# Performance work log

Hardware: AMD Instinct MI355X
Metric: run time of the kernel (lower is better)

Reference implementation:

```python
import jax, jax.numpy as jnp
import numpy as np

B, S, D, F, E, K, T = 4, 2048, 1024, 4096, 8, 2, 64


def setup_inputs() -> dict:
    key = jax.random.key(0)
    ks = jax.random.split(key, 12)
    s = 0.02
    return {
        "inputs": jax.random.normal(ks[0], (B, S, D), jnp.float32),
        "task_param": jax.random.normal(ks[1], (B, S, T), jnp.float32),
        "alpha": jnp.array(0.5, jnp.float32),
        "Wg_in": jax.random.normal(ks[2], (D, E), jnp.float32) * s,
        "bg_in": jnp.zeros((E,), jnp.float32),
        "Wg_task": jax.random.normal(ks[3], (T, E), jnp.float32) * s,
        "bg_task": jnp.zeros((E,), jnp.float32),
        "W1": jax.random.normal(ks[4], (E, D, F), jnp.float32) * s,
        "b1": jnp.zeros((E, F), jnp.float32),
        "W2": jax.random.normal(ks[5], (E, F, D), jnp.float32) * s,
        "b2": jnp.zeros((E, D), jnp.float32),
    }


def reference(inputs, task_param, alpha, Wg_in, bg_in, Wg_task, bg_task, W1, b1, W2, b2):
    dtype = inputs.dtype
    # blended gate logits: (1-alpha)*input_gate(x) + alpha*task_gate(task)
    gate_logits = (1.0 - alpha) * (jnp.einsum("bsd,de->bse", inputs, Wg_in) + bg_in) \
                + alpha * (jnp.einsum("bst,te->bse", task_param, Wg_task) + bg_task)
    # top-k expert selection (torch.topk: sorted descending)
    topk_vals, selected = jax.lax.top_k(gate_logits, K)  # [B,S,K]
    # aux load-balancing loss
    weights_softmax = jax.nn.softmax(gate_logits.astype(jnp.float32), axis=-1).astype(dtype)
    average_weight = weights_softmax.mean(axis=(0, 1))                 # [E]
    onehot = jax.nn.one_hot(selected, E, dtype=jnp.float32)            # [B,S,K,E]
    average_count = onehot.sum(axis=2).mean(axis=(0, 1)).astype(dtype) # [E]
    l_aux = jnp.mean(average_weight * average_count) * E
    # combine weights: softmax over the K selected logits, scattered to expert slots
    w = jax.nn.softmax(topk_vals.astype(jnp.float32), axis=-1).astype(dtype)  # [B,S,K]
    combine = jnp.einsum("bsk,bske->bse", w.astype(jnp.float32), onehot).astype(dtype)  # [B,S,E]
    # dense dispatch/combine (math-equivalent to boolean-mask gather/scatter loop)
    results = jnp.zeros_like(inputs)
    for e in range(E):
        h = jax.nn.gelu(jnp.einsum("bsd,df->bsf", inputs, W1[e]) + b1[e])
        y = jnp.einsum("bsf,fd->bsd", h, W2[e]) + b2[e]
        results = results + combine[..., e:e + 1] * y
    return (results, l_aux.astype(jnp.float32))
```

## Files before the change

kernel.cpp:

```cpp
#include <hip/hip_runtime.h>

#define NTOK 8192
#define DDIM 1024
#define FDIM 4096
#define NEXP 8
#define TDIM 64
#define MAXBLK 72

#define H_OFF   (1u<<20)
#define W1B_OFF (H_OFF + 134217728u)
#define W2B_OFF (W1B_OFF + 67108864u)
#define XB_OFF  (W2B_OFF + 67108864u)
#define FULL_WS (XB_OFF + 16777216u)

typedef __bf16 bf16x8 __attribute__((ext_vector_type(8)));
typedef unsigned short u16x8 __attribute__((ext_vector_type(8)));
typedef unsigned short u16x4 __attribute__((ext_vector_type(4)));
typedef float f32x4 __attribute__((ext_vector_type(4)));

__device__ __forceinline__ float gelu_tanh(float h) {
  float u = 0.7978845608028654f * (h + 0.044715f * h * h * h);
  float e = __expf(2.0f * u);
  return 0.5f * h * (2.0f - 2.0f / (e + 1.0f));
}

__device__ __forceinline__ void glds16(const void* g, void* l) {
  __builtin_amdgcn_global_load_lds((const __attribute__((address_space(1))) void*)g,
                                   (__attribute__((address_space(3))) void*)l, 16, 0, 0);
}

__global__ __launch_bounds__(256) void gate_kernel(
    const float* __restrict__ x, const float* __restrict__ task,
    const float* __restrict__ alpha_p,
    const float* __restrict__ Wg_in, const float* __restrict__ bg_in,
    const float* __restrict__ Wg_task, const float* __restrict__ bg_task,
    int* __restrict__ cnt, float* __restrict__ wsum,
    int* __restrict__ tok_list, float* __restrict__ wt_list)
{
  __shared__ float s_wsum[NEXP];
  int tid = threadIdx.x;
  if (tid < NEXP) s_wsum[tid] = 0.0f;
  __syncthreads();

  int lane = tid & 63;
  int wid  = tid >> 6;
  int tok  = blockIdx.x * 4 + wid;
  float a  = alpha_p[0];

  const float* xr = x + (size_t)tok * DDIM;
  float accd[8] = {0,0,0,0,0,0,0,0};
#pragma unroll
  for (int i = 0; i < DDIM/64; ++i) {
    int d = lane + 64*i;
    float xv = xr[d];
    f32x4 wa = *(const f32x4*)(Wg_in + (size_t)d*8);
    f32x4 wb = *(const f32x4*)(Wg_in + (size_t)d*8 + 4);
#pragma unroll
    for (int j = 0; j < 4; ++j) {
      accd[j]   = fmaf(xv, wa[j], accd[j]);
      accd[4+j] = fmaf(xv, wb[j], accd[4+j]);
    }
  }
  float part[8];
  {
    int d = lane;
    float tv = task[(size_t)tok*TDIM + d];
    f32x4 wa = *(const f32x4*)(Wg_task + (size_t)d*8);
    f32x4 wb = *(const f32x4*)(Wg_task + (size_t)d*8 + 4);
#pragma unroll
    for (int j = 0; j < 4; ++j) {
      part[j]   = (1.0f-a)*accd[j]   + a*(tv*wa[j]);
      part[4+j] = (1.0f-a)*accd[4+j] + a*(tv*wb[j]);
    }
  }
#pragma unroll
  for (int e = 0; e < 8; ++e) {
#pragma unroll
    for (int m = 1; m < 64; m <<= 1) part[e] += __shfl_xor(part[e], m);
  }

  if (lane == 0) {
    float lg[8];
#pragma unroll
    for (int e = 0; e < 8; ++e) lg[e] = part[e] + (1.0f-a)*bg_in[e] + a*bg_task[e];
    int e0 = 0;
#pragma unroll
    for (int e = 1; e < 8; ++e) if (lg[e] > lg[e0]) e0 = e;
    int e1 = (e0 == 0) ? 1 : 0;
#pragma unroll
    for (int e = 0; e < 8; ++e) if (e != e0 && lg[e] > lg[e1]) e1 = e;
    float mx = lg[0];
#pragma unroll
    for (int e = 1; e < 8; ++e) mx = fmaxf(mx, lg[e]);
    float p[8], s = 0.0f;
#pragma unroll
    for (int e = 0; e < 8; ++e) { p[e] = __expf(lg[e] - mx); s += p[e]; }
    float inv = 1.0f / s;
#pragma unroll
    for (int e = 0; e < 8; ++e) atomicAdd(&s_wsum[e], p[e] * inv);
    float p1 = __expf(lg[e1] - lg[e0]);
    float w0 = 1.0f / (1.0f + p1);
    float w1 = p1 * w0;
    int pos0 = atomicAdd(&cnt[e0], 1);
    tok_list[e0*NTOK + pos0] = tok; wt_list[e0*NTOK + pos0] = w0;
    int pos1 = atomicAdd(&cnt[e1], 1);
    tok_list[e1*NTOK + pos1] = tok; wt_list[e1*NTOK + pos1] = w1;
  }
  __syncthreads();
  if (tid < NEXP) atomicAdd(&wsum[tid], s_wsum[tid]);
}

__global__ void finalize_kernel(const int* __restrict__ cnt, const float* __restrict__ wsum,
                                int* __restrict__ offs, float* __restrict__ laux,
                                int* __restrict__ blk_e, int* __restrict__ blk_m)
{
  if (threadIdx.x == 0) {
    int o = 0; float l = 0.0f; int nb = 0;
    for (int e = 0; e < NEXP; ++e) {
      offs[e] = o;
      for (int m0 = 0; m0 < cnt[e]; m0 += 256) {
        if (nb < MAXBLK) { blk_e[nb] = e; blk_m[nb] = m0; ++nb; }
      }
      l += (wsum[e] * (1.0f/NTOK)) * ((float)cnt[e] * (1.0f/NTOK));
      o += cnt[e];
    }
    for (; nb < MAXBLK; ++nb) blk_e[nb] = -1;
    *laux = l;
  }
}

__global__ __launch_bounds__(256) void prep_x(const float* __restrict__ X,
                                              unsigned short* __restrict__ Xb)
{
  size_t i = ((size_t)blockIdx.x*256 + threadIdx.x)*8;
  f32x4 a = *(const f32x4*)(X + i);
  f32x4 b = *(const f32x4*)(X + i + 4);
  u16x8 v;
#pragma unroll
  for (int j = 0; j < 4; ++j) {
    v[j]   = __builtin_bit_cast(unsigned short, (__bf16)a[j]);
    v[4+j] = __builtin_bit_cast(unsigned short, (__bf16)b[j]);
  }
  *(u16x8*)(Xb + i) = v;
}

template<bool PERM>
__global__ __launch_bounds__(256) void prep_w(const float* __restrict__ W,
                                              unsigned short* __restrict__ Wb,
                                              int N, int NKB, int NJ)
{
  int kb = blockIdx.x, J = blockIdx.y, e = blockIdx.z;
  int K = NKB*64;
  __shared__ unsigned short t[64*264];
  int tid = threadIdx.x;
  const float* src = W + ((size_t)e*K + (size_t)kb*64) * N + J*256;
  int k = tid >> 2, cg = tid & 3;
#pragma unroll
  for (int ii = 0; ii < 16; ++ii) {
    int n = cg*64 + ii*4;
    f32x4 v = *(const f32x4*)(src + (size_t)k*N + n);
    u16x4 b;
#pragma unroll
    for (int j = 0; j < 4; ++j) b[j] = __builtin_bit_cast(unsigned short, (__bf16)v[j]);
    *(u16x4*)&t[k*264 + n] = b;
  }
  __syncthreads();
  unsigned short* dst = Wb + ((size_t)(e*NJ + J)*NKB + kb)*16384;
#pragma unroll
  for (int i = 0; i < 8; ++i) {
    int c = i*256 + tid;
    int r = c >> 3, cc = c & 7;
    u16x8 v;
#pragma unroll
    for (int j = 0; j < 8; ++j) {
      int kloc = ((cc ^ (r&7)) << 3) + j;
      if (PERM) kloc = ((kloc & 3) << 4) | (kloc >> 2);
      v[j] = t[kloc*264 + r];
    }
    *(u16x8*)(dst + c*8) = v;
  }
}


#define STAGE(sa, sb, ks) do {                                              \
  _Pragma("unroll")                                                         \
  for (int i_ = 0; i_ < 4; ++i_) {                                          \
    glds16(asrc[i_] + (size_t)(ks)*128, (char*)(sa) + dstoff[i_]);          \
    glds16(bsrc + (size_t)(ks)*32768 + i_*8192, (char*)(sb) + dstoff[i_]);  \
  }                                                                         \
} while (0)

#define COMPUTE(sa, sb) do {                                                \
  _Pragma("unroll")                                                         \
  for (int kk_ = 0; kk_ < 2; ++kk_) {                                       \
    int csw_ = ((kk_*4 + g) ^ (q & 7)) << 3;                                \
    bf16x8 bfv_[4];                                                         \
    _Pragma("unroll")                                                       \
    for (int ni_ = 0; ni_ < 4; ++ni_)                                       \
      bfv_[ni_] = *(const bf16x8*)&(sb)[(wc*64 + ni_*16 + q)*64 + csw_];    \
    _Pragma("unroll")                                                       \
    for (int mi_ = 0; mi_ < 8; ++mi_) {                                     \
      bf16x8 af_ = *(const bf16x8*)&(sa)[(wr*128 + mi_*16 + q)*64 + csw_];  \
      _Pragma("unroll")                                                     \
      for (int ni_ = 0; ni_ < 4; ++ni_)                                     \
        acc[mi_][ni_] = __builtin_amdgcn_mfma_f32_16x16x32_bf16(af_, bfv_[ni_], acc[mi_][ni_], 0, 0, 0); \
    }                                                                       \
  }                                                                         \
} while (0)

__global__ __launch_bounds__(512) void gemm1_v4(
    const unsigned short* __restrict__ Xb, const unsigned short* __restrict__ W1b,
    const float* __restrict__ b1,
    const int* __restrict__ cnt, const int* __restrict__ offs,
    const int* __restrict__ tok_list,
    const int* __restrict__ blk_e, const int* __restrict__ blk_m,
    unsigned short* __restrict__ H)
{
  int e = blk_e[blockIdx.x];
  if (e < 0) return;
  int m0 = blk_m[blockIdx.x];
  int ce = cnt[e];
  int off = offs[e];
  int J = blockIdx.y;

  __shared__ __align__(16) unsigned short sA0[256*64], sB0[256*64];
  __shared__ __align__(16) unsigned short sA1[256*64], sB1[256*64];
  __shared__ int s_tok[256];

  int tid = threadIdx.x;
  if (tid < 256) {
    int idx = m0 + tid;
    s_tok[tid] = tok_list[e*NTOK + ((idx < ce) ? idx : (ce-1))];
  }
  __syncthreads();

  int w = tid >> 6, l = tid & 63;
  int wr = w >> 2, wc = w & 3;
  int q = l & 15, g = l >> 4;

  const char* asrc[4];
  int dstoff[4];
#pragma unroll
  for (int i = 0; i < 4; ++i) {
    int c = i*512 + tid;
    int r = c >> 3, cc = c & 7;
    asrc[i]  = (const char*)(Xb + (size_t)s_tok[r]*DDIM) + ((cc ^ (r&7)) << 4);
    dstoff[i] = c*16;
  }
  const char* bsrc = (const char*)W1b + ((size_t)(e*16 + J)*16)*32768 + (size_t)tid*16;

  f32x4 acc[8][4];
#pragma unroll
  for (int mi = 0; mi < 8; ++mi)
#pragma unroll
    for (int ni = 0; ni < 4; ++ni) acc[mi][ni] = (f32x4){0.f,0.f,0.f,0.f};

  STAGE(sA0, sB0, 0);
  asm volatile("s_waitcnt vmcnt(0)" ::: "memory");
  __builtin_amdgcn_s_barrier();

#define NK1 (DDIM/64)
  for (int ks = 0; ks < NK1; ks += 2) {
    STAGE(sA1, sB1, ks+1);
    COMPUTE(sA0, sB0);
    asm volatile("s_waitcnt vmcnt(0)" ::: "memory");
    __builtin_amdgcn_s_barrier();
    if (ks + 2 < NK1) STAGE(sA0, sB0, ks+2);
    COMPUTE(sA1, sB1);
    asm volatile("s_waitcnt vmcnt(0)" ::: "memory");
    __builtin_amdgcn_s_barrier();
  }

  int n0 = J*256;
  float bias[4];
#pragma unroll
  for (int ni = 0; ni < 4; ++ni) bias[ni] = b1[(size_t)e*FDIM + n0 + wc*64 + ni*16 + q];
#pragma unroll
  for (int mi = 0; mi < 8; ++mi) {
#pragma unroll
    for (int j = 0; j < 4; ++j) {
      int r = wr*128 + mi*16 + g*4 + j;
      if (m0 + r >= ce) continue;
      u16x4 hv;
#pragma unroll
      for (int ni = 0; ni < 4; ++ni) {
        float h = acc[mi][ni][j] + bias[ni];
        hv[ni] = __builtin_bit_cast(unsigned short, (__bf16)gelu_tanh(h));
      }
      *(u16x4*)&H[(size_t)(off + m0 + r)*FDIM + n0 + wc*64 + q*4] = hv;
    }
  }
}

__global__ __launch_bounds__(512) void gemm2_v4(
    const unsigned short* __restrict__ H, const unsigned short* __restrict__ W2b,
    const float* __restrict__ b2,
    const int* __restrict__ cnt, const int* __restrict__ offs,
    const int* __restrict__ tok_list, const float* __restrict__ wt_list,
    const int* __restrict__ blk_e, const int* __restrict__ blk_m,
    float* __restrict__ out)
{
  int e = blk_e[blockIdx.x];
  if (e < 0) return;
  int m0 = blk_m[blockIdx.x];
  int ce = cnt[e];
  int off = offs[e];
  int J = blockIdx.y;

  __shared__ __align__(16) unsigned short sA0[256*64], sB0[256*64];
  __shared__ __align__(16) unsigned short sA1[256*64], sB1[256*64];
  __shared__ int   s_tok[256];
  __shared__ float s_wt[256];

  int tid = threadIdx.x;
  if (tid < 256) {
    int idx = m0 + tid;
    int cidx = (idx < ce) ? idx : (ce-1);
    s_tok[tid] = tok_list[e*NTOK + cidx];
    s_wt[tid]  = (idx < ce) ? wt_list[e*NTOK + cidx] : 0.0f;
  }
  __syncthreads();

  int w = tid >> 6, l = tid & 63;
  int wr = w >> 2, wc = w & 3;
  int q = l & 15, g = l >> 4;

  const char* asrc[4];
  int dstoff[4];
#pragma unroll
  for (int i = 0; i < 4; ++i) {
    int c = i*512 + tid;
    int r = c >> 3, cc = c & 7;
    int rr = (m0 + r < ce) ? r : (ce-1-m0);
    asrc[i]  = (const char*)(H + (size_t)(off + m0 + rr)*FDIM) + ((cc ^ (r&7)) << 4);
    dstoff[i] = c*16;
  }
  const char* bsrc = (const char*)W2b + ((size_t)(e*4 + J)*64)*32768 + (size_t)tid*16;

  f32x4 acc[8][4];
#pragma unroll
  for (int mi = 0; mi < 8; ++mi)
#pragma unroll
    for (int ni = 0; ni < 4; ++ni) acc[mi][ni] = (f32x4){0.f,0.f,0.f,0.f};

  STAGE(sA0, sB0, 0);
  asm volatile("s_waitcnt vmcnt(0)" ::: "memory");
  __builtin_amdgcn_s_barrier();

#define NK2 (FDIM/64)
  for (int ks = 0; ks < NK2; ks += 2) {
    STAGE(sA1, sB1, ks+1);
    COMPUTE(sA0, sB0);
    asm volatile("s_waitcnt vmcnt(0)" ::: "memory");
    __builtin_amdgcn_s_barrier();
    if (ks + 2 < NK2) STAGE(sA0, sB0, ks+2);
    COMPUTE(sA1, sB1);
    asm volatile("s_waitcnt vmcnt(0)" ::: "memory");
    __builtin_amdgcn_s_barrier();
  }

  int n0 = J*256;
  float bias[4];
#pragma unroll
  for (int ni = 0; ni < 4; ++ni) bias[ni] = b2[(size_t)e*DDIM + n0 + wc*64 + ni*16 + q];
#pragma unroll
  for (int mi = 0; mi < 8; ++mi) {
#pragma unroll
    for (int j = 0; j < 4; ++j) {
      int r = wr*128 + mi*16 + g*4 + j;
      if (m0 + r >= ce) continue;
      int tok = s_tok[r];
      float wt = s_wt[r];
      float* orow = out + (size_t)tok * DDIM;
#pragma unroll
      for (int ni = 0; ni < 4; ++ni) {
        float y = acc[mi][ni][j] + bias[ni];
        unsafeAtomicAdd(&orow[n0 + wc*64 + ni*16 + q], wt * y);
      }
    }
  }
}

extern "C" void kernel_launch(void* const* d_in, const int* in_sizes, int n_in,
                              void* d_out, int out_size, void* d_ws, size_t ws_size,
                              hipStream_t stream)
{
  const float* x       = (const float*)d_in[0];
  const float* task    = (const float*)d_in[1];
  const float* alpha   = (const float*)d_in[2];
  const float* Wg_in   = (const float*)d_in[3];
  const float* bg_in   = (const float*)d_in[4];
  const float* Wg_task = (const float*)d_in[5];
  const float* bg_task = (const float*)d_in[6];
  const float* W1      = (const float*)d_in[7];
  const float* b1      = (const float*)d_in[8];
  const float* W2      = (const float*)d_in[9];
  const float* b2      = (const float*)d_in[10];
  float* out = (float*)d_out;

  char* ws = (char*)d_ws;
  int*   cnt      = (int*)(ws + 0);
  float* wsum     = (float*)(ws + 32);
  int*   offs     = (int*)(ws + 64);
  int*   blk_e    = (int*)(ws + 128);
  int*   blk_m    = (int*)(ws + 512);
  int*   tok_list = (int*)(ws + 4096);
  float* wt_list  = (float*)(ws + 4096 + NTOK*NEXP*4);
  unsigned short* H   = (unsigned short*)(ws + H_OFF);
  unsigned short* W1b = (unsigned short*)(ws + W1B_OFF);
  unsigned short* W2b = (unsigned short*)(ws + W2B_OFF);
  unsigned short* Xb  = (unsigned short*)(ws + XB_OFF);

  hipMemsetAsync(d_out, 0, (size_t)out_size * sizeof(float), stream);
  hipMemsetAsync(ws, 0, 128, stream);
  gate_kernel<<<NTOK/4, 256, 0, stream>>>(x, task, alpha, Wg_in, bg_in, Wg_task, bg_task,
                                          cnt, wsum, tok_list, wt_list);
  finalize_kernel<<<1, 64, 0, stream>>>(cnt, wsum, offs, out + (size_t)NTOK*DDIM, blk_e, blk_m);
  prep_x<<<NTOK*DDIM/2048, 256, 0, stream>>>(x, Xb);
  prep_w<false><<<dim3(16, 16, NEXP), 256, 0, stream>>>(W1, W1b, FDIM, 16, 16);
  prep_w<true ><<<dim3(64,  4, NEXP), 256, 0, stream>>>(W2, W2b, DDIM, 64, 4);
  gemm1_v4<<<dim3(MAXBLK, FDIM/256), 512, 0, stream>>>(Xb, W1b, b1, cnt, offs, tok_list,
                                                       blk_e, blk_m, H);
  gemm2_v4<<<dim3(MAXBLK, DDIM/256), 512, 0, stream>>>(H, W2b, b2, cnt, offs, tok_list, wt_list,
                                                       blk_e, blk_m, out);
}
```

Baseline: 821.8 us.

## Switch expert GEMMs to 4-stage K=32 pipeline with split-K for GEMM2

Both grouped GEMMs move from a double-buffered K=64 loop that waits for all loads each step to a four-buffer ring of K=32 tiles, using partial vmcnt waits so up to three stages stay in flight. The weight pre-pack and the A-tile gather are re-laid out so two rows share one swizzled 64-element LDS line. The kernels also raise wave priority around the MFMA bursts and swap grid axes so blocks sharing a row tile launch together. GEMM2 gains a split-K of 2 along F, doubling the block count for better CU occupancy at the cost of twice as many atomic adds to the output.

```diff
diff --git a/kernel.cpp b/kernel.cpp
--- a/kernel.cpp
+++ b/kernel.cpp
@@ -28,6 +28,11 @@
   __builtin_amdgcn_global_load_lds((const __attribute__((address_space(1))) void*)g,
                                    (__attribute__((address_space(3))) void*)l, 16, 0, 0);
 }
+
+#define VM8() asm volatile("s_waitcnt vmcnt(8)" ::: "memory")
+#define VM4() asm volatile("s_waitcnt vmcnt(4)" ::: "memory")
+#define VM0() asm volatile("s_waitcnt vmcnt(0)" ::: "memory")
+#define BAR() __builtin_amdgcn_s_barrier()
 
 __global__ __launch_bounds__(256) void gate_kernel(
     const float* __restrict__ x, const float* __restrict__ task,
@@ -168,47 +173,53 @@
   unsigned short* dst = Wb + ((size_t)(e*NJ + J)*NKB + kb)*16384;
 #pragma unroll
   for (int i = 0; i < 8; ++i) {
-    int c = i*256 + tid;
-    int r = c >> 3, cc = c & 7;
+    int c2 = i*256 + tid;
+    int cl = c2 & 1023;
+    int h  = c2 >> 10;
+    int R  = cl >> 3, dp = cl & 7;
+    int d  = dp ^ (R & 7);
+    int nloc = (R<<1) | (d>>2);
+    int pbase = h*32 + (d&3)*8;
     u16x8 v;
 #pragma unroll
     for (int j = 0; j < 8; ++j) {
-      int kloc = ((cc ^ (r&7)) << 3) + j;
-      if (PERM) kloc = ((kloc & 3) << 4) | (kloc >> 2);
-      v[j] = t[kloc*264 + r];
-    }
-    *(u16x8*)(dst + c*8) = v;
-  }
-}
-
-
-#define STAGE(sa, sb, ks) do {                                              \
-  _Pragma("unroll")                                                         \
-  for (int i_ = 0; i_ < 4; ++i_) {                                          \
-    glds16(asrc[i_] + (size_t)(ks)*128, (char*)(sa) + dstoff[i_]);          \
-    glds16(bsrc + (size_t)(ks)*32768 + i_*8192, (char*)(sb) + dstoff[i_]);  \
-  }                                                                         \
+      int v64 = pbase + j;
+      int kl  = PERM ? (((v64 & 3) << 4) | (v64 >> 2)) : v64;
+      v[j] = t[kl*264 + nloc];
+    }
+    *(u16x8*)(dst + (size_t)c2*8) = v;
+  }
+}
+
+
+#define STAGE(bufbase, t) do {                                                \
+  char* sa__ = ldsb + (bufbase);                                              \
+  _Pragma("unroll")                                                           \
+  for (int i_ = 0; i_ < 2; ++i_) {                                            \
+    glds16(asrc[i_] + (size_t)(t)*64, sa__ + dstoff[i_]);                     \
+    glds16(bsrc + (size_t)(t)*16384 + i_*8192, sa__ + 16384 + dstoff[i_]);    \
+  }                                                                           \
 } while (0)
 
-#define COMPUTE(sa, sb) do {                                                \
-  _Pragma("unroll")                                                         \
-  for (int kk_ = 0; kk_ < 2; ++kk_) {                                       \
-    int csw_ = ((kk_*4 + g) ^ (q & 7)) << 3;                                \
-    bf16x8 bfv_[4];                                                         \
-    _Pragma("unroll")                                                       \
-    for (int ni_ = 0; ni_ < 4; ++ni_)                                       \
-      bfv_[ni_] = *(const bf16x8*)&(sb)[(wc*64 + ni_*16 + q)*64 + csw_];    \
-    _Pragma("unroll")                                                       \
-    for (int mi_ = 0; mi_ < 8; ++mi_) {                                     \
-      bf16x8 af_ = *(const bf16x8*)&(sa)[(wr*128 + mi_*16 + q)*64 + csw_];  \
-      _Pragma("unroll")                                                     \
-      for (int ni_ = 0; ni_ < 4; ++ni_)                                     \
-        acc[mi_][ni_] = __builtin_amdgcn_mfma_f32_16x16x32_bf16(af_, bfv_[ni_], acc[mi_][ni_], 0, 0, 0); \
-    }                                                                       \
-  }                                                                         \
+#define COMPUTE(bufbase) do {                                                 \
+  const unsigned short* sa_ = (const unsigned short*)(ldsb + (bufbase));      \
+  const unsigned short* sb_ = sa_ + 8192;                                     \
+  bf16x8 bfv_[4];                                                             \
+  _Pragma("unroll")                                                           \
+  for (int ni_ = 0; ni_ < 4; ++ni_)                                           \
+    bfv_[ni_] = *(const bf16x8*)&sb_[boff0 + ni_*512];                        \
+  __builtin_amdgcn_s_setprio(1);                                              \
+  _Pragma("unroll")                                                           \
+  for (int mi_ = 0; mi_ < 8; ++mi_) {                                         \
+    bf16x8 af_ = *(const bf16x8*)&sa_[aoff0 + mi_*512];                       \
+    _Pragma("unroll")                                                         \
+    for (int ni_ = 0; ni_ < 4; ++ni_)                                         \
+      acc[mi_][ni_] = __builtin_amdgcn_mfma_f32_16x16x32_bf16(af_, bfv_[ni_], acc[mi_][ni_], 0, 0, 0); \
+  }                                                                           \
+  __builtin_amdgcn_s_setprio(0);                                              \
 } while (0)
 
-__global__ __launch_bounds__(512) void gemm1_v4(
+__global__ __launch_bounds__(512) void gemm1_v5(
     const unsigned short* __restrict__ Xb, const unsigned short* __restrict__ W1b,
     const float* __restrict__ b1,
     const int* __restrict__ cnt, const int* __restrict__ offs,
@@ -216,15 +227,14 @@
     const int* __restrict__ blk_e, const int* __restrict__ blk_m,
     unsigned short* __restrict__ H)
 {
-  int e = blk_e[blockIdx.x];
+  int e = blk_e[blockIdx.y];
   if (e < 0) return;
-  int m0 = blk_m[blockIdx.x];
+  int m0 = blk_m[blockIdx.y];
   int ce = cnt[e];
   int off = offs[e];
-  int J = blockIdx.y;
-
-  __shared__ __align__(16) unsigned short sA0[256*64], sB0[256*64];
-  __shared__ __align__(16) unsigned short sA1[256*64], sB1[256*64];
+  int J = blockIdx.x;
+
+  __shared__ __align__(16) char ldsb[131072];
   __shared__ int s_tok[256];
 
   int tid = threadIdx.x;
@@ -234,20 +244,29 @@
   }
   __syncthreads();
 
-  int w = tid >> 6, l = tid & 63;
+  int l = tid & 63, w = tid >> 6;
   int wr = w >> 2, wc = w & 3;
   int q = l & 15, g = l >> 4;
 
-  const char* asrc[4];
-  int dstoff[4];
-#pragma unroll
-  for (int i = 0; i < 4; ++i) {
+  const char* asrc[2];
+  int dstoff[2];
+#pragma unroll
+  for (int i = 0; i < 2; ++i) {
     int c = i*512 + tid;
-    int r = c >> 3, cc = c & 7;
-    asrc[i]  = (const char*)(Xb + (size_t)s_tok[r]*DDIM) + ((cc ^ (r&7)) << 4);
+    int R = c >> 3, dp = c & 7;
+    int d = dp ^ (R & 7);
+    int r = (R << 1) | (d >> 2);
+    int kc = d & 3;
+    asrc[i] = (const char*)(Xb + (size_t)s_tok[r]*DDIM) + kc*16;
     dstoff[i] = c*16;
   }
-  const char* bsrc = (const char*)W1b + ((size_t)(e*16 + J)*16)*32768 + (size_t)tid*16;
+  const char* bsrc = (const char*)W1b + (size_t)((e*16 + J)*32) * 16384 + (size_t)tid*16;
+
+  int rowA = wr*128 + q, rowB = wc*64 + q;
+  int RA = rowA >> 1, RB = rowB >> 1;
+  int dq = ((q & 1) << 2) | g;
+  const int aoff0 = RA*64 + (dq ^ (RA & 7))*8;
+  const int boff0 = RB*64 + (dq ^ (RB & 7))*8;
 
   f32x4 acc[8][4];
 #pragma unroll
@@ -255,21 +274,17 @@
 #pragma unroll
     for (int ni = 0; ni < 4; ++ni) acc[mi][ni] = (f32x4){0.f,0.f,0.f,0.f};
 
-  STAGE(sA0, sB0, 0);
-  asm volatile("s_waitcnt vmcnt(0)" ::: "memory");
-  __builtin_amdgcn_s_barrier();
-
-#define NK1 (DDIM/64)
-  for (int ks = 0; ks < NK1; ks += 2) {
-    STAGE(sA1, sB1, ks+1);
-    COMPUTE(sA0, sB0);
-    asm volatile("s_waitcnt vmcnt(0)" ::: "memory");
-    __builtin_amdgcn_s_barrier();
-    if (ks + 2 < NK1) STAGE(sA0, sB0, ks+2);
-    COMPUTE(sA1, sB1);
-    asm volatile("s_waitcnt vmcnt(0)" ::: "memory");
-    __builtin_amdgcn_s_barrier();
-  }
+#define NT1 (DDIM/32)
+  STAGE(0, 0); STAGE(32768, 1); STAGE(65536, 2);
+  VM8(); BAR();
+  for (int t = 0; t < NT1-3; ++t) {
+    STAGE(((t+3)&3)*32768, t+3);
+    COMPUTE((t&3)*32768);
+    VM8(); BAR();
+  }
+  COMPUTE(((NT1-3)&3)*32768); VM4(); BAR();
+  COMPUTE(((NT1-2)&3)*32768); VM0(); BAR();
+  COMPUTE(((NT1-1)&3)*32768);
 
   int n0 = J*256;
   float bias[4];
@@ -292,7 +307,7 @@
   }
 }
 
-__global__ __launch_bounds__(512) void gemm2_v4(
+__global__ __launch_bounds__(512) void gemm2_v5(
     const unsigned short* __restrict__ H, const unsigned short* __restrict__ W2b,
     const float* __restrict__ b2,
     const int* __restrict__ cnt, const int* __restrict__ offs,
@@ -300,15 +315,15 @@
     const int* __restrict__ blk_e, const int* __restrict__ blk_m,
     float* __restrict__ out)
 {
-  int e = blk_e[blockIdx.x];
+  int e = blk_e[blockIdx.y];
   if (e < 0) return;
-  int m0 = blk_m[blockIdx.x];
+  int m0 = blk_m[blockIdx.y];
   int ce = cnt[e];
   int off = offs[e];
-  int J = blockIdx.y;
-
-  __shared__ __align__(16) unsigned short sA0[256*64], sB0[256*64];
-  __shared__ __align__(16) unsigned short sA1[256*64], sB1[256*64];
+  int J = blockIdx.x;
+  int s = blockIdx.z;
+
+  __shared__ __align__(16) char ldsb[131072];
   __shared__ int   s_tok[256];
   __shared__ float s_wt[256];
 
@@ -321,21 +336,30 @@
   }
   __syncthreads();
 
-  int w = tid >> 6, l = tid & 63;
+  int l = tid & 63, w = tid >> 6;
   int wr = w >> 2, wc = w & 3;
   int q = l & 15, g = l >> 4;
 
-  const char* asrc[4];
-  int dstoff[4];
-#pragma unroll
-  for (int i = 0; i < 4; ++i) {
+  const char* asrc[2];
+  int dstoff[2];
+#pragma unroll
+  for (int i = 0; i < 2; ++i) {
     int c = i*512 + tid;
-    int r = c >> 3, cc = c & 7;
+    int R = c >> 3, dp = c & 7;
+    int d = dp ^ (R & 7);
+    int r = (R << 1) | (d >> 2);
+    int kc = d & 3;
     int rr = (m0 + r < ce) ? r : (ce-1-m0);
-    asrc[i]  = (const char*)(H + (size_t)(off + m0 + rr)*FDIM) + ((cc ^ (r&7)) << 4);
+    asrc[i] = (const char*)(H + (size_t)(off + m0 + rr)*FDIM) + kc*16 + s*4096;
     dstoff[i] = c*16;
   }
-  const char* bsrc = (const char*)W2b + ((size_t)(e*4 + J)*64)*32768 + (size_t)tid*16;
+  const char* bsrc = (const char*)W2b + (size_t)((e*4 + J)*128 + s*64) * 16384 + (size_t)tid*16;
+
+  int rowA = wr*128 + q, rowB = wc*64 + q;
+  int RA = rowA >> 1, RB = rowB >> 1;
+  int dq = ((q & 1) << 2) | g;
+  const int aoff0 = RA*64 + (dq ^ (RA & 7))*8;
+  const int boff0 = RB*64 + (dq ^ (RB & 7))*8;
 
   f32x4 acc[8][4];
 #pragma unroll
@@ -343,26 +367,23 @@
 #pragma unroll
     for (int ni = 0; ni < 4; ++ni) acc[mi][ni] = (f32x4){0.f,0.f,0.f,0.f};
 
-  STAGE(sA0, sB0, 0);
-  asm volatile("s_waitcnt vmcnt(0)" ::: "memory");
-  __builtin_amdgcn_s_barrier();
-
-#define NK2 (FDIM/64)
-  for (int ks = 0; ks < NK2; ks += 2) {
-    STAGE(sA1, sB1, ks+1);
-    COMPUTE(sA0, sB0);
-    asm volatile("s_waitcnt vmcnt(0)" ::: "memory");
-    __builtin_amdgcn_s_barrier();
-    if (ks + 2 < NK2) STAGE(sA0, sB0, ks+2);
-    COMPUTE(sA1, sB1);
-    asm volatile("s_waitcnt vmcnt(0)" ::: "memory");
-    __builtin_amdgcn_s_barrier();
-  }
+#define NT2 (FDIM/32/2)
+  STAGE(0, 0); STAGE(32768, 1); STAGE(65536, 2);
+  VM8(); BAR();
+  for (int t = 0; t < NT2-3; ++t) {
+    STAGE(((t+3)&3)*32768, t+3);
+    COMPUTE((t&3)*32768);
+    VM8(); BAR();
+  }
+  COMPUTE(((NT2-3)&3)*32768); VM4(); BAR();
+  COMPUTE(((NT2-2)&3)*32768); VM0(); BAR();
+  COMPUTE(((NT2-1)&3)*32768);
 
   int n0 = J*256;
   float bias[4];
 #pragma unroll
-  for (int ni = 0; ni < 4; ++ni) bias[ni] = b2[(size_t)e*DDIM + n0 + wc*64 + ni*16 + q];
+  for (int ni = 0; ni < 4; ++ni)
+    bias[ni] = (s == 0) ? b2[(size_t)e*DDIM + n0 + wc*64 + ni*16 + q] : 0.0f;
 #pragma unroll
   for (int mi = 0; mi < 8; ++mi) {
 #pragma unroll
@@ -419,8 +440,8 @@
   prep_x<<<NTOK*DDIM/2048, 256, 0, stream>>>(x, Xb);
   prep_w<false><<<dim3(16, 16, NEXP), 256, 0, stream>>>(W1, W1b, FDIM, 16, 16);
   prep_w<true ><<<dim3(64,  4, NEXP), 256, 0, stream>>>(W2, W2b, DDIM, 64, 4);
-  gemm1_v4<<<dim3(MAXBLK, FDIM/256), 512, 0, stream>>>(Xb, W1b, b1, cnt, offs, tok_list,
-                                                       blk_e, blk_m, H);
-  gemm2_v4<<<dim3(MAXBLK, DDIM/256), 512, 0, stream>>>(H, W2b, b2, cnt, offs, tok_list, wt_list,
-                                                       blk_e, blk_m, out);
-}
+  gemm1_v5<<<dim3(16, MAXBLK), 512, 0, stream>>>(Xb, W1b, b1, cnt, offs, tok_list,
+                                                 blk_e, blk_m, H);
+  gemm2_v5<<<dim3(4, MAXBLK, 2), 512, 0, stream>>>(H, W2b, b2, cnt, offs, tok_list, wt_list,
+                                                   blk_e, blk_m, out);
+}
```

After: 911.6 us. 1.11x slower.

## Split gemm2 K dimension across two blocks and pre-gather expert tokens

Applied to the files above, without the earlier changes.

The second expert GEMM now splits the F reduction into two halves across a new grid z dimension. The two halves are summed through the existing atomic adds, and only the first half adds the bias. This doubles the block count to improve CU occupancy when few expert tiles exist, at the cost of twice the atomic traffic to the output. When the workspace is large enough, a new gather kernel also writes bf16 copies of the routed tokens contiguously in expert order, so gemm1 reads rows linearly instead of through an indirect token lookup.

```diff
diff --git a/kernel.cpp b/kernel.cpp
--- a/kernel.cpp
+++ b/kernel.cpp
@@ -12,6 +12,7 @@
 #define W2B_OFF (W1B_OFF + 67108864u)
 #define XB_OFF  (W2B_OFF + 67108864u)
 #define FULL_WS (XB_OFF + 16777216u)
+#define WS_BIG  (XB_OFF + 33554432u)
 
 typedef __bf16 bf16x8 __attribute__((ext_vector_type(8)));
 typedef unsigned short u16x8 __attribute__((ext_vector_type(8)));
@@ -144,6 +145,30 @@
   *(u16x8*)(Xb + i) = v;
 }
 
+__global__ __launch_bounds__(256) void prep_gather(
+    const float* __restrict__ X,
+    const int* __restrict__ offs, const int* __restrict__ tok_list,
+    unsigned short* __restrict__ Xg)
+{
+  int tid = threadIdx.x;
+  int sl = blockIdx.x*2 + (tid >> 7);
+  int e = 0;
+#pragma unroll
+  for (int k = 1; k < NEXP; ++k) if (sl >= offs[k]) e = k;
+  int tok = tok_list[e*NTOK + (sl - offs[e])];
+  int c8 = (tid & 127) * 8;
+  const float* src = X + (size_t)tok * DDIM + c8;
+  f32x4 a = *(const f32x4*)(src);
+  f32x4 b = *(const f32x4*)(src + 4);
+  u16x8 v;
+#pragma unroll
+  for (int j = 0; j < 4; ++j) {
+    v[j]   = __builtin_bit_cast(unsigned short, (__bf16)a[j]);
+    v[4+j] = __builtin_bit_cast(unsigned short, (__bf16)b[j]);
+  }
+  *(u16x8*)(Xg + (size_t)sl * DDIM + c8) = v;
+}
+
 template<bool PERM>
 __global__ __launch_bounds__(256) void prep_w(const float* __restrict__ W,
                                               unsigned short* __restrict__ Wb,
@@ -173,9 +198,9 @@
     u16x8 v;
 #pragma unroll
     for (int j = 0; j < 8; ++j) {
-      int kloc = ((cc ^ (r&7)) << 3) + j;
-      if (PERM) kloc = ((kloc & 3) << 4) | (kloc >> 2);
-      v[j] = t[kloc*264 + r];
+      int v64 = (cc ^ (r&7))*8 + j;
+      int kl  = PERM ? (((v64 & 3) << 4) | (v64 >> 2)) : v64;
+      v[j] = t[kl*264 + r];
     }
     *(u16x8*)(dst + c*8) = v;
   }
@@ -208,8 +233,9 @@
   }                                                                         \
 } while (0)
 
-__global__ __launch_bounds__(512) void gemm1_v4(
-    const unsigned short* __restrict__ Xb, const unsigned short* __restrict__ W1b,
+template<bool LIN>
+__global__ __launch_bounds__(512) void gemm1_v8(
+    const unsigned short* __restrict__ Xsrc, const unsigned short* __restrict__ W1b,
     const float* __restrict__ b1,
     const int* __restrict__ cnt, const int* __restrict__ offs,
     const int* __restrict__ tok_list,
@@ -228,11 +254,13 @@
   __shared__ int s_tok[256];
 
   int tid = threadIdx.x;
-  if (tid < 256) {
-    int idx = m0 + tid;
-    s_tok[tid] = tok_list[e*NTOK + ((idx < ce) ? idx : (ce-1))];
-  }
-  __syncthreads();
+  if (!LIN) {
+    if (tid < 256) {
+      int idx = m0 + tid;
+      s_tok[tid] = tok_list[e*NTOK + ((idx < ce) ? idx : (ce-1))];
+    }
+    __syncthreads();
+  }
 
   int w = tid >> 6, l = tid & 63;
   int wr = w >> 2, wc = w & 3;
@@ -244,7 +272,12 @@
   for (int i = 0; i < 4; ++i) {
     int c = i*512 + tid;
     int r = c >> 3, cc = c & 7;
-    asrc[i]  = (const char*)(Xb + (size_t)s_tok[r]*DDIM) + ((cc ^ (r&7)) << 4);
+    if (LIN) {
+      int rr = (m0 + r < ce) ? r : (ce-1-m0);
+      asrc[i] = (const char*)(Xsrc + (size_t)(off + m0 + rr)*DDIM) + ((cc ^ (r&7)) << 4);
+    } else {
+      asrc[i] = (const char*)(Xsrc + (size_t)s_tok[r]*DDIM) + ((cc ^ (r&7)) << 4);
+    }
     dstoff[i] = c*16;
   }
   const char* bsrc = (const char*)W1b + ((size_t)(e*16 + J)*16)*32768 + (size_t)tid*16;
@@ -292,7 +325,7 @@
   }
 }
 
-__global__ __launch_bounds__(512) void gemm2_v4(
+__global__ __launch_bounds__(512) void gemm2_v8(
     const unsigned short* __restrict__ H, const unsigned short* __restrict__ W2b,
     const float* __restrict__ b2,
     const int* __restrict__ cnt, const int* __restrict__ offs,
@@ -306,6 +339,7 @@
   int ce = cnt[e];
   int off = offs[e];
   int J = blockIdx.y;
+  int s = blockIdx.z;
 
   __shared__ __align__(16) unsigned short sA0[256*64], sB0[256*64];
   __shared__ __align__(16) unsigned short sA1[256*64], sB1[256*64];
@@ -332,10 +366,10 @@
     int c = i*512 + tid;
     int r = c >> 3, cc = c & 7;
     int rr = (m0 + r < ce) ? r : (ce-1-m0);
-    asrc[i]  = (const char*)(H + (size_t)(off + m0 + rr)*FDIM) + ((cc ^ (r&7)) << 4);
+    asrc[i]  = (const char*)(H + (size_t)(off + m0 + rr)*FDIM) + ((cc ^ (r&7)) << 4) + s*4096;
     dstoff[i] = c*16;
   }
-  const char* bsrc = (const char*)W2b + ((size_t)(e*4 + J)*64)*32768 + (size_t)tid*16;
+  const char* bsrc = (const char*)W2b + ((size_t)(e*4 + J)*64 + s*32)*32768 + (size_t)tid*16;
 
   f32x4 acc[8][4];
 #pragma unroll
@@ -347,7 +381,7 @@
   asm volatile("s_waitcnt vmcnt(0)" ::: "memory");
   __builtin_amdgcn_s_barrier();
 
-#define NK2 (FDIM/64)
+#define NK2 (FDIM/64/2)
   for (int ks = 0; ks < NK2; ks += 2) {
     STAGE(sA1, sB1, ks+1);
     COMPUTE(sA0, sB0);
@@ -362,7 +396,8 @@
   int n0 = J*256;
   float bias[4];
 #pragma unroll
-  for (int ni = 0; ni < 4; ++ni) bias[ni] = b2[(size_t)e*DDIM + n0 + wc*64 + ni*16 + q];
+  for (int ni = 0; ni < 4; ++ni)
+    bias[ni] = (s == 0) ? b2[(size_t)e*DDIM + n0 + wc*64 + ni*16 + q] : 0.0f;
 #pragma unroll
   for (int mi = 0; mi < 8; ++mi) {
 #pragma unroll
@@ -410,17 +445,25 @@
   unsigned short* W1b = (unsigned short*)(ws + W1B_OFF);
   unsigned short* W2b = (unsigned short*)(ws + W2B_OFF);
   unsigned short* Xb  = (unsigned short*)(ws + XB_OFF);
+  unsigned short* Xg  = (unsigned short*)(ws + XB_OFF);
 
   hipMemsetAsync(d_out, 0, (size_t)out_size * sizeof(float), stream);
   hipMemsetAsync(ws, 0, 128, stream);
   gate_kernel<<<NTOK/4, 256, 0, stream>>>(x, task, alpha, Wg_in, bg_in, Wg_task, bg_task,
                                           cnt, wsum, tok_list, wt_list);
   finalize_kernel<<<1, 64, 0, stream>>>(cnt, wsum, offs, out + (size_t)NTOK*DDIM, blk_e, blk_m);
-  prep_x<<<NTOK*DDIM/2048, 256, 0, stream>>>(x, Xb);
   prep_w<false><<<dim3(16, 16, NEXP), 256, 0, stream>>>(W1, W1b, FDIM, 16, 16);
   prep_w<true ><<<dim3(64,  4, NEXP), 256, 0, stream>>>(W2, W2b, DDIM, 64, 4);
-  gemm1_v4<<<dim3(MAXBLK, FDIM/256), 512, 0, stream>>>(Xb, W1b, b1, cnt, offs, tok_list,
-                                                       blk_e, blk_m, H);
-  gemm2_v4<<<dim3(MAXBLK, DDIM/256), 512, 0, stream>>>(H, W2b, b2, cnt, offs, tok_list, wt_list,
-                                                       blk_e, blk_m, out);
-}
+
+  if (ws_size >= (size_t)WS_BIG) {
+    prep_gather<<<NTOK, 256, 0, stream>>>(x, offs, tok_list, Xg);
+    gemm1_v8<true><<<dim3(MAXBLK, FDIM/256), 512, 0, stream>>>(Xg, W1b, b1, cnt, offs,
+                                                               tok_list, blk_e, blk_m, H);
+  } else {
+    prep_x<<<NTOK*DDIM/2048, 256, 0, stream>>>(x, Xb);
+    gemm1_v8<false><<<dim3(MAXBLK, FDIM/256), 512, 0, stream>>>(Xb, W1b, b1, cnt, offs,
+                                                                tok_list, blk_e, blk_m, H);
+  }
+  gemm2_v8<<<dim3(MAXBLK, DDIM/256, 2), 512, 0, stream>>>(H, W2b, b2, cnt, offs, tok_list,
+                                                          wt_list, blk_e, blk_m, out);
+}
```

New measurement: 850.0 us. 3.4% more time.

## Pre-gather tokens into tiled layout, shrink K-tiles, split-K gemm2 for occupancy

Applied to the files above, without the earlier changes.

Replaces the flat bf16 conversion of X with a kernel that gathers routed tokens into pre-swizzled, tile-contiguous blocks. Both GEMMs can then stage A and B with fully contiguous global-to-LDS loads. K-tiles drop from 64 to 32, cutting LDS per block and allowing launch_bounds(512,4) for higher occupancy. GEMM1 writes H directly in the tiled layout GEMM2 consumes, and GEMM2 is split along K into two halves that accumulate through the existing atomics, doubling grid parallelism. The cost is twice as many barrier-synchronised K iterations, an extra gather pass over X, and twice as many atomic adds in the gemm2 epilogue.

```diff
diff --git a/kernel.cpp b/kernel.cpp
--- a/kernel.cpp
+++ b/kernel.cpp
@@ -7,11 +7,11 @@
 #define TDIM 64
 #define MAXBLK 72
 
-#define H_OFF   (1u<<20)
-#define W1B_OFF (H_OFF + 134217728u)
-#define W2B_OFF (W1B_OFF + 67108864u)
-#define XB_OFF  (W2B_OFF + 67108864u)
-#define FULL_WS (XB_OFF + 16777216u)
+#define HG_OFF   1048576u
+#define W1B_OFF  (HG_OFF + 150994944u)
+#define W2B_OFF  (W1B_OFF + 67108864u)
+#define XGT_OFF  (W2B_OFF + 67108864u)
+#define WS_NEED  (XGT_OFF + 37748736u)
 
 typedef __bf16 bf16x8 __attribute__((ext_vector_type(8)));
 typedef unsigned short u16x8 __attribute__((ext_vector_type(8)));
@@ -28,6 +28,9 @@
   __builtin_amdgcn_global_load_lds((const __attribute__((address_space(1))) void*)g,
                                    (__attribute__((address_space(3))) void*)l, 16, 0, 0);
 }
+
+#define VM0() asm volatile("s_waitcnt vmcnt(0)" ::: "memory")
+#define SBAR() __syncthreads()
 
 __global__ __launch_bounds__(256) void gate_kernel(
     const float* __restrict__ x, const float* __restrict__ task,
@@ -129,21 +132,6 @@
   }
 }
 
-__global__ __launch_bounds__(256) void prep_x(const float* __restrict__ X,
-                                              unsigned short* __restrict__ Xb)
-{
-  size_t i = ((size_t)blockIdx.x*256 + threadIdx.x)*8;
-  f32x4 a = *(const f32x4*)(X + i);
-  f32x4 b = *(const f32x4*)(X + i + 4);
-  u16x8 v;
-#pragma unroll
-  for (int j = 0; j < 4; ++j) {
-    v[j]   = __builtin_bit_cast(unsigned short, (__bf16)a[j]);
-    v[4+j] = __builtin_bit_cast(unsigned short, (__bf16)b[j]);
-  }
-  *(u16x8*)(Xb + i) = v;
-}
-
 template<bool PERM>
 __global__ __launch_bounds__(256) void prep_w(const float* __restrict__ W,
                                               unsigned short* __restrict__ Wb,
@@ -165,89 +153,129 @@
     *(u16x4*)&t[k*264 + n] = b;
   }
   __syncthreads();
-  unsigned short* dst = Wb + ((size_t)(e*NJ + J)*NKB + kb)*16384;
+  unsigned short* dst = Wb + ((size_t)(e*NJ + J)*NKB + kb) * 16384;
 #pragma unroll
   for (int i = 0; i < 8; ++i) {
-    int c = i*256 + tid;
-    int r = c >> 3, cc = c & 7;
+    int c2 = i*256 + tid;
+    int h  = c2 >> 10, cl = c2 & 1023;
+    int R  = cl >> 3, dp = cl & 7;
+    int d  = dp ^ (R & 7);
+    int n  = (R << 1) | (d >> 2);
+    int kb8 = (d & 3) * 8;
     u16x8 v;
 #pragma unroll
     for (int j = 0; j < 8; ++j) {
-      int kloc = ((cc ^ (r&7)) << 3) + j;
-      if (PERM) kloc = ((kloc & 3) << 4) | (kloc >> 2);
-      v[j] = t[kloc*264 + r];
-    }
-    *(u16x8*)(dst + c*8) = v;
-  }
-}
-
-
-#define STAGE(sa, sb, ks) do {                                              \
-  _Pragma("unroll")                                                         \
-  for (int i_ = 0; i_ < 4; ++i_) {                                          \
-    glds16(asrc[i_] + (size_t)(ks)*128, (char*)(sa) + dstoff[i_]);          \
-    glds16(bsrc + (size_t)(ks)*32768 + i_*8192, (char*)(sb) + dstoff[i_]);  \
-  }                                                                         \
-} while (0)
-
-#define COMPUTE(sa, sb) do {                                                \
-  _Pragma("unroll")                                                         \
-  for (int kk_ = 0; kk_ < 2; ++kk_) {                                       \
-    int csw_ = ((kk_*4 + g) ^ (q & 7)) << 3;                                \
-    bf16x8 bfv_[4];                                                         \
-    _Pragma("unroll")                                                       \
-    for (int ni_ = 0; ni_ < 4; ++ni_)                                       \
-      bfv_[ni_] = *(const bf16x8*)&(sb)[(wc*64 + ni_*16 + q)*64 + csw_];    \
-    _Pragma("unroll")                                                       \
-    for (int mi_ = 0; mi_ < 8; ++mi_) {                                     \
-      bf16x8 af_ = *(const bf16x8*)&(sa)[(wr*128 + mi_*16 + q)*64 + csw_];  \
-      _Pragma("unroll")                                                     \
-      for (int ni_ = 0; ni_ < 4; ++ni_)                                     \
-        acc[mi_][ni_] = __builtin_amdgcn_mfma_f32_16x16x32_bf16(af_, bfv_[ni_], acc[mi_][ni_], 0, 0, 0); \
-    }                                                                       \
-  }                                                                         \
-} while (0)
-
-__global__ __launch_bounds__(512) void gemm1_v4(
-    const unsigned short* __restrict__ Xb, const unsigned short* __restrict__ W1b,
-    const float* __restrict__ b1,
-    const int* __restrict__ cnt, const int* __restrict__ offs,
-    const int* __restrict__ tok_list,
+      int vv = h*32 + kb8 + j;
+      int sk = PERM ? (((vv & 3) << 4) | (vv >> 2)) : vv;
+      v[j] = t[sk*264 + n];
+    }
+    *(u16x8*)(dst + (size_t)c2*8) = v;
+  }
+}
+
+__global__ __launch_bounds__(256) void prep_gather_t(
+    const float* __restrict__ X,
+    const int* __restrict__ cnt, const int* __restrict__ tok_list,
     const int* __restrict__ blk_e, const int* __restrict__ blk_m,
-    unsigned short* __restrict__ H)
-{
-  int e = blk_e[blockIdx.x];
+    unsigned short* __restrict__ XgT)
+{
+  int kt = blockIdx.x, bi = blockIdx.y;
+  int e = blk_e[bi];
   if (e < 0) return;
-  int m0 = blk_m[blockIdx.x];
-  int ce = cnt[e];
-  int off = offs[e];
-  int J = blockIdx.y;
-
-  __shared__ __align__(16) unsigned short sA0[256*64], sB0[256*64];
-  __shared__ __align__(16) unsigned short sA1[256*64], sB1[256*64];
+  int m0 = blk_m[bi], ce = cnt[e];
   __shared__ int s_tok[256];
-
   int tid = threadIdx.x;
   if (tid < 256) {
     int idx = m0 + tid;
     s_tok[tid] = tok_list[e*NTOK + ((idx < ce) ? idx : (ce-1))];
   }
   __syncthreads();
-
+  unsigned short* dst = XgT + ((size_t)bi*32 + kt) * 8192;
+#pragma unroll
+  for (int i = 0; i < 4; ++i) {
+    int c = i*256 + tid;
+    int R = c >> 3, dp = c & 7;
+    int d = dp ^ (R & 7);
+    int row = (R << 1) | (d >> 2);
+    int kloc = (d & 3) * 8;
+    const float* src = X + (size_t)s_tok[row]*DDIM + kt*32 + kloc;
+    f32x4 a = *(const f32x4*)(src);
+    f32x4 b = *(const f32x4*)(src + 4);
+    u16x8 v;
+#pragma unroll
+    for (int j = 0; j < 4; ++j) {
+      v[j]   = __builtin_bit_cast(unsigned short, (__bf16)a[j]);
+      v[4+j] = __builtin_bit_cast(unsigned short, (__bf16)b[j]);
+    }
+    *(u16x8*)(dst + (size_t)c*8) = v;
+  }
+}
+
+
+#define STAGE(sa, sb, kt) do {                                                 \
+  glds16(abase + (size_t)(kt)*16384 + t16,        (char*)(sa) + t16);          \
+  glds16(abase + (size_t)(kt)*16384 + 8192 + t16, (char*)(sa) + 8192 + t16);   \
+  glds16(bbase + (size_t)(kt)*16384 + t16,        (char*)(sb) + t16);          \
+  glds16(bbase + (size_t)(kt)*16384 + 8192 + t16, (char*)(sb) + 8192 + t16);   \
+} while (0)
+
+#define COMPUTE(sa, sb) do {                                                   \
+  bf16x8 bfv_[4];                                                              \
+  _Pragma("unroll")                                                            \
+  for (int ni_ = 0; ni_ < 4; ++ni_)                                            \
+    bfv_[ni_] = *(const bf16x8*)&(sb)[boff0 + ni_*512];                        \
+  _Pragma("unroll")                                                            \
+  for (int mi_ = 0; mi_ < 8; ++mi_) {                                          \
+    bf16x8 af_ = *(const bf16x8*)&(sa)[aoff0 + mi_*512];                       \
+    _Pragma("unroll")                                                          \
+    for (int ni_ = 0; ni_ < 4; ++ni_)                                          \
+      acc[mi_][ni_] = __builtin_amdgcn_mfma_f32_16x16x32_bf16(                 \
+          af_, bfv_[ni_], acc[mi_][ni_], 0, 0, 0);                             \
+  }                                                                            \
+} while (0)
+
+#define KLOOP(NT) do {                                                         \
+  STAGE(sA0, sB0, 0);                                                          \
+  VM0(); SBAR();                                                               \
+  for (int kt = 0; kt < (NT); kt += 2) {                                       \
+    STAGE(sA1, sB1, kt+1);                                                     \
+    COMPUTE(sA0, sB0);                                                         \
+    VM0(); SBAR();                                                             \
+    if (kt + 2 < (NT)) STAGE(sA0, sB0, kt+2);                                  \
+    COMPUTE(sA1, sB1);                                                         \
+    VM0(); SBAR();                                                             \
+  }                                                                            \
+} while (0)
+
+__global__ __launch_bounds__(512, 4) void gemm1_v11(
+    const unsigned short* __restrict__ XgT, const unsigned short* __restrict__ W1b,
+    const float* __restrict__ b1,
+    const int* __restrict__ cnt,
+    const int* __restrict__ blk_e, const int* __restrict__ blk_m,
+    unsigned short* __restrict__ Hg)
+{
+  int J = blockIdx.x;
+  int bi = blockIdx.y;
+  int e = blk_e[bi];
+  if (e < 0) return;
+  int m0 = blk_m[bi];
+  int ce = cnt[e];
+
+  __shared__ __align__(16) unsigned short sA0[8192], sB0[8192], sA1[8192], sB1[8192];
+
+  int tid = threadIdx.x;
   int w = tid >> 6, l = tid & 63;
   int wr = w >> 2, wc = w & 3;
   int q = l & 15, g = l >> 4;
-
-  const char* asrc[4];
-  int dstoff[4];
-#pragma unroll
-  for (int i = 0; i < 4; ++i) {
-    int c = i*512 + tid;
-    int r = c >> 3, cc = c & 7;
-    asrc[i]  = (const char*)(Xb + (size_t)s_tok[r]*DDIM) + ((cc ^ (r&7)) << 4);
-    dstoff[i] = c*16;
-  }
-  const char* bsrc = (const char*)W1b + ((size_t)(e*16 + J)*16)*32768 + (size_t)tid*16;
+  const int t16 = tid * 16;
+
+  const char* abase = (const char*)XgT + (size_t)bi * 524288;
+  const char* bbase = (const char*)W1b + (size_t)(e*16 + J) * 32 * 16384;
+
+  int hq = q >> 1;
+  int swz = ((((q & 1) << 2) | g) ^ (hq & 7));
+  const int aoff0 = (wr*64 + hq)*64 + swz*8;
+  const int boff0 = (wc*32 + hq)*64 + swz*8;
 
   f32x4 acc[8][4];
 #pragma unroll
@@ -255,22 +283,12 @@
 #pragma unroll
     for (int ni = 0; ni < 4; ++ni) acc[mi][ni] = (f32x4){0.f,0.f,0.f,0.f};
 
-  STAGE(sA0, sB0, 0);
-  asm volatile("s_waitcnt vmcnt(0)" ::: "memory");
-  __builtin_amdgcn_s_barrier();
-
-#define NK1 (DDIM/64)
-  for (int ks = 0; ks < NK1; ks += 2) {
-    STAGE(sA1, sB1, ks+1);
-    COMPUTE(sA0, sB0);
-    asm volatile("s_waitcnt vmcnt(0)" ::: "memory");
-    __builtin_amdgcn_s_barrier();
-    if (ks + 2 < NK1) STAGE(sA0, sB0, ks+2);
-    COMPUTE(sA1, sB1);
-    asm volatile("s_waitcnt vmcnt(0)" ::: "memory");
-    __builtin_amdgcn_s_barrier();
-  }
-
+  KLOOP(DDIM/32);
+
+  int G = J*4 + wc;
+  int kt2g = G*2 + (q >> 3);
+  unsigned short* hgb = Hg + ((size_t)(bi*2 + (kt2g >> 6))*64 + (kt2g & 63)) * 8192;
+  int vh = (q & 7) >> 1;
   int n0 = J*256;
   float bias[4];
 #pragma unroll
@@ -287,28 +305,32 @@
         float h = acc[mi][ni][j] + bias[ni];
         hv[ni] = __builtin_bit_cast(unsigned short, (__bf16)gelu_tanh(h));
       }
-      *(u16x4*)&H[(size_t)(off + m0 + r)*FDIM + n0 + wc*64 + q*4] = hv;
-    }
-  }
-}
-
-__global__ __launch_bounds__(512) void gemm2_v4(
-    const unsigned short* __restrict__ H, const unsigned short* __restrict__ W2b,
+      int R = r >> 1;
+      int d = ((r & 1) << 2) | vh;
+      int cl = R*8 + (d ^ (R & 7));
+      *(u16x4*)&hgb[cl*8 + (q & 1)*4] = hv;
+    }
+  }
+}
+
+__global__ __launch_bounds__(512, 4) void gemm2_v11(
+    const unsigned short* __restrict__ Hg, const unsigned short* __restrict__ W2b,
     const float* __restrict__ b2,
     const int* __restrict__ cnt, const int* __restrict__ offs,
     const int* __restrict__ tok_list, const float* __restrict__ wt_list,
     const int* __restrict__ blk_e, const int* __restrict__ blk_m,
     float* __restrict__ out)
 {
-  int e = blk_e[blockIdx.x];
+  int Js = blockIdx.x;
+  int J = Js & 3, s = Js >> 2;
+  int bi = blockIdx.y;
+  int e = blk_e[bi];
   if (e < 0) return;
-  int m0 = blk_m[blockIdx.x];
+  int m0 = blk_m[bi];
   int ce = cnt[e];
   int off = offs[e];
-  int J = blockIdx.y;
-
-  __shared__ __align__(16) unsigned short sA0[256*64], sB0[256*64];
-  __shared__ __align__(16) unsigned short sA1[256*64], sB1[256*64];
+
+  __shared__ __align__(16) unsigned short sA0[8192], sB0[8192], sA1[8192], sB1[8192];
   __shared__ int   s_tok[256];
   __shared__ float s_wt[256];
 
@@ -324,18 +346,15 @@
   int w = tid >> 6, l = tid & 63;
   int wr = w >> 2, wc = w & 3;
   int q = l & 15, g = l >> 4;
-
-  const char* asrc[4];
-  int dstoff[4];
-#pragma unroll
-  for (int i = 0; i < 4; ++i) {
-    int c = i*512 + tid;
-    int r = c >> 3, cc = c & 7;
-    int rr = (m0 + r < ce) ? r : (ce-1-m0);
-    asrc[i]  = (const char*)(H + (size_t)(off + m0 + rr)*FDIM) + ((cc ^ (r&7)) << 4);
-    dstoff[i] = c*16;
-  }
-  const char* bsrc = (const char*)W2b + ((size_t)(e*4 + J)*64)*32768 + (size_t)tid*16;
+  const int t16 = tid * 16;
+
+  const char* abase = (const char*)Hg + ((size_t)(bi*2 + s) << 20);
+  const char* bbase = (const char*)W2b + (size_t)((e*4 + J)*128 + s*64) * 16384;
+
+  int hq = q >> 1;
+  int swz = ((((q & 1) << 2) | g) ^ (hq & 7));
+  const int aoff0 = (wr*64 + hq)*64 + swz*8;
+  const int boff0 = (wc*32 + hq)*64 + swz*8;
 
   f32x4 acc[8][4];
 #pragma unroll
@@ -343,26 +362,13 @@
 #pragma unroll
     for (int ni = 0; ni < 4; ++ni) acc[mi][ni] = (f32x4){0.f,0.f,0.f,0.f};
 
-  STAGE(sA0, sB0, 0);
-  asm volatile("s_waitcnt vmcnt(0)" ::: "memory");
-  __builtin_amdgcn_s_barrier();
-
-#define NK2 (FDIM/64)
-  for (int ks = 0; ks < NK2; ks += 2) {
-    STAGE(sA1, sB1, ks+1);
-    COMPUTE(sA0, sB0);
-    asm volatile("s_waitcnt vmcnt(0)" ::: "memory");
-    __builtin_amdgcn_s_barrier();
-    if (ks + 2 < NK2) STAGE(sA0, sB0, ks+2);
-    COMPUTE(sA1, sB1);
-    asm volatile("s_waitcnt vmcnt(0)" ::: "memory");
-    __builtin_amdgcn_s_barrier();
-  }
+  KLOOP(FDIM/32/2);
 
   int n0 = J*256;
   float bias[4];
 #pragma unroll
-  for (int ni = 0; ni < 4; ++ni) bias[ni] = b2[(size_t)e*DDIM + n0 + wc*64 + ni*16 + q];
+  for (int ni = 0; ni < 4; ++ni)
+    bias[ni] = (s == 0) ? b2[(size_t)e*DDIM + n0 + wc*64 + ni*16 + q] : 0.0f;
 #pragma unroll
   for (int mi = 0; mi < 8; ++mi) {
 #pragma unroll
@@ -406,21 +412,22 @@
   int*   blk_m    = (int*)(ws + 512);
   int*   tok_list = (int*)(ws + 4096);
   float* wt_list  = (float*)(ws + 4096 + NTOK*NEXP*4);
-  unsigned short* H   = (unsigned short*)(ws + H_OFF);
+  unsigned short* Hg  = (unsigned short*)(ws + HG_OFF);
   unsigned short* W1b = (unsigned short*)(ws + W1B_OFF);
   unsigned short* W2b = (unsigned short*)(ws + W2B_OFF);
-  unsigned short* Xb  = (unsigned short*)(ws + XB_OFF);
+  unsigned short* XgT = (unsigned short*)(ws + XGT_OFF);
 
   hipMemsetAsync(d_out, 0, (size_t)out_size * sizeof(float), stream);
   hipMemsetAsync(ws, 0, 128, stream);
   gate_kernel<<<NTOK/4, 256, 0, stream>>>(x, task, alpha, Wg_in, bg_in, Wg_task, bg_task,
                                           cnt, wsum, tok_list, wt_list);
   finalize_kernel<<<1, 64, 0, stream>>>(cnt, wsum, offs, out + (size_t)NTOK*DDIM, blk_e, blk_m);
-  prep_x<<<NTOK*DDIM/2048, 256, 0, stream>>>(x, Xb);
+
   prep_w<false><<<dim3(16, 16, NEXP), 256, 0, stream>>>(W1, W1b, FDIM, 16, 16);
   prep_w<true ><<<dim3(64,  4, NEXP), 256, 0, stream>>>(W2, W2b, DDIM, 64, 4);
-  gemm1_v4<<<dim3(MAXBLK, FDIM/256), 512, 0, stream>>>(Xb, W1b, b1, cnt, offs, tok_list,
-                                                       blk_e, blk_m, H);
-  gemm2_v4<<<dim3(MAXBLK, DDIM/256), 512, 0, stream>>>(H, W2b, b2, cnt, offs, tok_list, wt_list,
-                                                       blk_e, blk_m, out);
-}
+  prep_gather_t<<<dim3(32, MAXBLK), 256, 0, stream>>>(x, cnt, tok_list, blk_e, blk_m, XgT);
+
+  gemm1_v11<<<dim3(16, MAXBLK), 512, 0, stream>>>(XgT, W1b, b1, cnt, blk_e, blk_m, Hg);
+  gemm2_v11<<<dim3(8, MAXBLK), 512, 0, stream>>>(Hg, W2b, b2, cnt, offs, tok_list, wt_list,
+                                                 blk_e, blk_m, out);
+}
```

Measured after the change: 2.549 ms. 210% more time.
